# Performance work log

Measured on AMD Instinct MI355X. Metric: run time of the kernel, lower is better.

Reference implementation:

```python
import jax, jax.numpy as jnp
import numpy as np

B, S, D, H = 4, 2048, 1024, 16
DK = D // H
SCALE = 1.0 / np.float32(np.sqrt(DK))


def setup_inputs() -> dict:
    key = jax.random.key(0)
    ks = jax.random.split(key, 11)
    w = lambda k: (jax.random.normal(k, (D, D), jnp.float32) * 0.02)
    b = lambda k: (jax.random.normal(k, (D,), jnp.float32) * 0.02)
    return {
        "Q": jax.random.normal(ks[0], (B, S, D), jnp.float32),
        "K": jax.random.normal(ks[1], (B, S, D), jnp.float32),
        "V": jax.random.normal(ks[2], (B, S, D), jnp.float32),
        "Wq": w(ks[3]), "bq": b(ks[4]),
        "Wk": w(ks[5]), "bk": b(ks[6]),
        "Wv": w(ks[7]), "bv": b(ks[8]),
        "Wo": w(ks[9]), "bo": b(ks[10]),
        # causal mask, broadcast over batch and heads: [1,1,S,S]
        "mask": jnp.tril(jnp.ones((1, 1, S, S), dtype=bool)),
    }


def reference(Q, K, V, Wq, bq, Wk, bk, Wv, bv, Wo, bo, mask):
    def proj(x, W, bias):
        # [B,S,D] -> [B,H,S,DK]
        return (x @ W + bias).reshape(B, S, H, DK).transpose(0, 2, 1, 3)

    q = proj(Q, Wq, bq)
    k = proj(K, Wk, bk)
    v = proj(V, Wv, bv)
    scores = jnp.einsum("bhqd,bhkd->bhqk", q, k) * SCALE  # [B,H,S,S]
    scores = jnp.where(mask, scores, jnp.float32(-1e9))
    attn = jax.nn.softmax(scores, axis=-1)
    out = jnp.einsum("bhqk,bhkd->bhqd", attn, v)  # [B,H,S,DK]
    out = out.transpose(0, 2, 1, 3).reshape(B, S, D)
    return out @ Wo + bo
```

## Files before the change

kernel.cpp:

```cpp
#include <hip/hip_runtime.h>
#include <hip/hip_bf16.h>
#include <stdint.h>

#define BB 4
#define SS 2048
#define DD 1024
#define HH 16
#define DKK 64
#define MM (BB * SS)

typedef __hip_bfloat16 bf16;
typedef __attribute__((ext_vector_type(8))) short frag8;
typedef __attribute__((ext_vector_type(4))) float f32x4;

#define GLDS16(g, l)                                                        \
  __builtin_amdgcn_global_load_lds(                                         \
      (const __attribute__((address_space(1))) void*)(g),                   \
      (__attribute__((address_space(3))) void*)(l), 16, 0, 0)

#define MFMA __builtin_amdgcn_mfma_f32_16x16x32_bf16

__device__ __forceinline__ unsigned short f2bu(float f) {
  __hip_bfloat16 h = __float2bfloat16(f);
  return *reinterpret_cast<unsigned short*>(&h);
}

struct WtArgs {
  const float* s[3];
  unsigned short* d[3];
};
__global__ __launch_bounds__(256) void wtrans_kernel(WtArgs a) {
  const float* __restrict__ W = a.s[blockIdx.z];
  unsigned short* __restrict__ Wt = a.d[blockIdx.z];
  __shared__ float t[64][68];
  const int n0 = blockIdx.x * 64, k0 = blockIdx.y * 64;
  const int tid = threadIdx.x;
#pragma unroll
  for (int it = 0; it < 4; ++it) {
    const int kk = it * 16 + (tid >> 4);
    const int nn = (tid & 15) * 4;
    const float4 v = *(const float4*)&W[(size_t)(k0 + kk) * DD + n0 + nn];
    *(float4*)&t[kk][nn] = v;
  }
  __syncthreads();
#pragma unroll
  for (int it = 0; it < 2; ++it) {
    const int n = it * 32 + (tid >> 3);
    const int c = tid & 7;
    frag8 pk;
#pragma unroll
    for (int j = 0; j < 8; ++j) pk[j] = (short)f2bu(t[c * 8 + j][n]);
    *(frag8*)&Wt[(size_t)(n0 + n) * DD + k0 + c * 8] = pk;
  }
}

template <int A_BF16, int OUT_MODE>
__global__ __launch_bounds__(256) void gemm_kernel(
    const void* __restrict__ Av, const unsigned short* __restrict__ Wt,
    const float* __restrict__ bias, void* __restrict__ outv, float oscale) {
  constexpr int K = DD;
  __shared__ unsigned short Bs[128 * 64];
  __shared__ unsigned short As[128 * 64];
  const int tid = threadIdx.x;
  const int wave = tid >> 6, lane = tid & 63, quad = lane >> 4, l15 = lane & 15;
  const int wr = wave >> 1, wc = wave & 1;
  const int m0 = blockIdx.y * 128, n0 = blockIdx.x * 128;

  f32x4 acc[4][4] = {};

  for (int k0 = 0; k0 < K; k0 += 64) {
#pragma unroll
    for (int c = 0; c < 4; ++c) {
      const int row = c * 32 + wave * 8 + (lane >> 3);
      const int gc = ((lane & 7) ^ (row & 7)) * 8;
      const unsigned short* g = &Wt[(size_t)(n0 + row) * K + k0 + gc];
      unsigned off = __builtin_amdgcn_readfirstlane(
          (unsigned)((c * 32 + wave * 8) * 128));
      GLDS16(g, (char*)&Bs[0] + off);
    }
    if (A_BF16) {
      const unsigned short* A = (const unsigned short*)Av;
#pragma unroll
      for (int c = 0; c < 4; ++c) {
        const int row = c * 32 + wave * 8 + (lane >> 3);
        const int gc = ((lane & 7) ^ (row & 7)) * 8;
        const unsigned short* g = &A[(size_t)(m0 + row) * K + k0 + gc];
        unsigned off = __builtin_amdgcn_readfirstlane(
            (unsigned)((c * 32 + wave * 8) * 128));
        GLDS16(g, (char*)&As[0] + off);
      }
    } else {
      const float* A = (const float*)Av;
#pragma unroll
      for (int it = 0; it < 4; ++it) {
        const int row = it * 32 + (tid >> 3);
        const int c = tid & 7;
        const float4 v0 = *(const float4*)&A[(size_t)(m0 + row) * K + k0 + c * 8];
        const float4 v1 =
            *(const float4*)&A[(size_t)(m0 + row) * K + k0 + c * 8 + 4];
        frag8 pk;
        pk[0] = (short)f2bu(v0.x); pk[1] = (short)f2bu(v0.y);
        pk[2] = (short)f2bu(v0.z); pk[3] = (short)f2bu(v0.w);
        pk[4] = (short)f2bu(v1.x); pk[5] = (short)f2bu(v1.y);
        pk[6] = (short)f2bu(v1.z); pk[7] = (short)f2bu(v1.w);
        *(frag8*)&As[row * 64 + ((c ^ (row & 7)) * 8)] = pk;
      }
    }
    __syncthreads();

#pragma unroll
    for (int s = 0; s < 2; ++s) {
      frag8 af[4], bfr[4];
#pragma unroll
      for (int mi = 0; mi < 4; ++mi)
        af[mi] = *(const frag8*)
            &As[(wr * 64 + mi * 16 + l15) * 64 + (((s * 4 + quad) ^ (l15 & 7)) * 8)];
#pragma unroll
      for (int ni = 0; ni < 4; ++ni)
        bfr[ni] = *(const frag8*)
            &Bs[(wc * 64 + ni * 16 + l15) * 64 + (((s * 4 + quad) ^ (l15 & 7)) * 8)];
#pragma unroll
      for (int mi = 0; mi < 4; ++mi)
#pragma unroll
        for (int ni = 0; ni < 4; ++ni)
          acc[mi][ni] = MFMA(af[mi], bfr[ni], acc[mi][ni], 0, 0, 0);
    }
    __syncthreads();
  }

#pragma unroll
  for (int mi = 0; mi < 4; ++mi) {
#pragma unroll
    for (int ni = 0; ni < 4; ++ni) {
#pragma unroll
      for (int r = 0; r < 4; ++r) {
        const int grow = m0 + wr * 64 + mi * 16 + quad * 4 + r;
        const int gcol = n0 + wc * 64 + ni * 16 + l15;
        const float val = (acc[mi][ni][r] + bias[gcol]) * oscale;
        if (OUT_MODE == 2) {
          ((float*)outv)[(size_t)grow * DD + gcol] = val;
        } else {
          const int b = grow / SS, s = grow % SS;
          const int h = gcol / DKK, dk = gcol % DKK;
          unsigned short* o = (unsigned short*)outv;
          if (OUT_MODE == 0)
            o[(((size_t)(b * HH + h)) * SS + s) * DKK + dk] = f2bu(val);
          else
            o[(((size_t)(b * HH + h)) * DKK + dk) * SS + s] = f2bu(val);
        }
      }
    }
  }
}

__global__ __launch_bounds__(256) void fattn_kernel(
    const unsigned short* __restrict__ q, const unsigned short* __restrict__ k,
    const unsigned short* __restrict__ vt, unsigned short* __restrict__ ctx) {
  __shared__ unsigned short Ks[2][64 * 64];
  __shared__ unsigned short Vs[2][64 * 64];
  __shared__ unsigned short P_lds[4][16][36];
  const int tid = threadIdx.x;
  const int wave = tid >> 6, lane = tid & 63, quad = lane >> 4, l15 = lane & 15;
  const int bh = blockIdx.x & 63;
  const int tp = blockIdx.x >> 6;
  const size_t qkb = (size_t)bh * SS * DKK;
  const size_t vtb = (size_t)bh * DKK * SS;
  const int b = bh / HH, h = bh % HH;

  frag8 ones;
#pragma unroll
  for (int s = 0; s < 8; ++s) ones[s] = (short)0x3F80;

  auto stage = [&](int buf, int jt) {
#pragma unroll
    for (int c = 0; c < 2; ++c) {
      const int row = wave * 16 + c * 8 + (lane >> 3);
      const int gc = ((lane & 7) ^ (row & 7)) * 8;
      const unsigned short* g = &k[qkb + (size_t)(jt * 64 + row) * DKK + gc];
      unsigned off = __builtin_amdgcn_readfirstlane(
          (unsigned)(buf * 8192 + (wave * 16 + c * 8) * 128));
      GLDS16(g, (char*)&Ks[0][0] + off);
    }
#pragma unroll
    for (int c = 0; c < 2; ++c) {
      const int row = wave * 16 + c * 8 + (lane >> 3);
      const int gc = ((lane & 7) ^ (row & 7)) * 8;
      const unsigned short* g = &vt[vtb + (size_t)row * SS + jt * 64 + gc];
      unsigned off = __builtin_amdgcn_readfirstlane(
          (unsigned)(buf * 8192 + (wave * 16 + c * 8) * 128));
      GLDS16(g, (char*)&Vs[0][0] + off);
    }
  };

  for (int half = 0; half < 2; ++half) {
    const int t = half ? (31 - tp) : tp;
    const int q0 = t * 64 + wave * 16;

    const frag8 aq0 =
        *(const frag8*)&q[qkb + (size_t)(q0 + l15) * DKK + quad * 8];
    const frag8 aq1 =
        *(const frag8*)&q[qkb + (size_t)(q0 + l15) * DKK + 32 + quad * 8];

    f32x4 oacc[4] = {};
    f32x4 lacc = {};

    const int nT = t + 1;
    stage(0, 0);
    __syncthreads();

    for (int jt = 0; jt < nT; ++jt) {
      const int p = jt & 1;
      if (jt + 1 < nT) stage(1 - p, jt + 1);
      const bool diag = (jt == t);

#pragma unroll
      for (int jsub = 0; jsub < 2; ++jsub) {
        f32x4 sc[2];
#pragma unroll
        for (int g = 0; g < 2; ++g) {
          const int row = jsub * 32 + g * 16 + l15;
          const frag8 kf0 =
              *(const frag8*)&Ks[p][row * 64 + ((quad ^ (l15 & 7)) * 8)];
          const frag8 kf1 =
              *(const frag8*)&Ks[p][row * 64 + (((4 + quad) ^ (l15 & 7)) * 8)];
          f32x4 z = {};
          z = MFMA(aq0, kf0, z, 0, 0, 0);
          sc[g] = MFMA(aq1, kf1, z, 0, 0, 0);
        }
        float p0[4], p1[4];
        if (diag) {
          const int jg = jt * 64 + jsub * 32;
#pragma unroll
          for (int r = 0; r < 4; ++r) {
            const int ig = q0 + quad * 4 + r;
            p0[r] = (jg + l15 <= ig) ? __expf(sc[0][r]) : 0.f;
            p1[r] = (jg + 16 + l15 <= ig) ? __expf(sc[1][r]) : 0.f;
          }
        } else {
#pragma unroll
          for (int r = 0; r < 4; ++r) {
            p0[r] = __expf(sc[0][r]);
            p1[r] = __expf(sc[1][r]);
          }
        }
#pragma unroll
        for (int r = 0; r < 4; ++r) {
          P_lds[wave][quad * 4 + r][l15] = f2bu(p0[r]);
          P_lds[wave][quad * 4 + r][16 + l15] = f2bu(p1[r]);
        }
        const frag8 pa = *(const frag8*)&P_lds[wave][l15][quad * 8];
#pragma unroll
        for (int c = 0; c < 4; ++c) {
          const int vrow = c * 16 + l15;
          const int chunk = ((jsub * 4 + quad) ^ (l15 & 7));
          const frag8 vf = *(const frag8*)&Vs[p][vrow * 64 + chunk * 8];
          oacc[c] = MFMA(pa, vf, oacc[c], 0, 0, 0);
        }
        lacc = MFMA(pa, ones, lacc, 0, 0, 0);
      }
      __syncthreads();
    }

#pragma unroll
    for (int r = 0; r < 4; ++r) {
      const float inv = 1.f / lacc[r];
      const int ig = q0 + quad * 4 + r;
#pragma unroll
      for (int c = 0; c < 4; ++c)
        ctx[((size_t)(b * SS + ig)) * DD + h * DKK + c * 16 + l15] =
            f2bu(oacc[c][r] * inv);
    }
  }
}

extern "C" void kernel_launch(void* const* d_in, const int* in_sizes, int n_in,
                              void* d_out, int out_size, void* d_ws,
                              size_t ws_size, hipStream_t stream) {
  const float* Q = (const float*)d_in[0];
  const float* K = (const float*)d_in[1];
  const float* V = (const float*)d_in[2];
  const float* Wq = (const float*)d_in[3];
  const float* bq = (const float*)d_in[4];
  const float* Wk = (const float*)d_in[5];
  const float* bk = (const float*)d_in[6];
  const float* Wv = (const float*)d_in[7];
  const float* bv = (const float*)d_in[8];
  const float* Wo = (const float*)d_in[9];
  const float* bo = (const float*)d_in[10];

  const size_t NE = (size_t)MM * DD;
  unsigned short* ctx = (unsigned short*)d_ws;
  unsigned short* qp = ctx + NE;
  unsigned short* kp = qp + NE;
  unsigned short* vtp = kp + NE;
  unsigned short* Wqt = ctx;
  unsigned short* Wkt = ctx + 1048576;
  unsigned short* Wvt = ctx + 2097152;
  unsigned short* Wot = qp;

  const dim3 gg(DD / 128, MM / 128);

  WtArgs wa1;
  wa1.s[0] = Wq; wa1.s[1] = Wk; wa1.s[2] = Wv;
  wa1.d[0] = Wqt; wa1.d[1] = Wkt; wa1.d[2] = Wvt;
  wtrans_kernel<<<dim3(16, 16, 3), 256, 0, stream>>>(wa1);

  gemm_kernel<0, 0><<<gg, 256, 0, stream>>>((const void*)Q, Wqt, bq, qp,
                                            0.125f);
  gemm_kernel<0, 0><<<gg, 256, 0, stream>>>((const void*)K, Wkt, bk, kp, 1.f);
  gemm_kernel<0, 1><<<gg, 256, 0, stream>>>((const void*)V, Wvt, bv, vtp, 1.f);

  fattn_kernel<<<dim3(BB * HH * 16), 256, 0, stream>>>(qp, kp, vtp, ctx);

  WtArgs wa2;
  wa2.s[0] = Wo; wa2.d[0] = Wot;
  wa2.s[1] = Wo; wa2.d[1] = Wot;
  wa2.s[2] = Wo; wa2.d[2] = Wot;
  wtrans_kernel<<<dim3(16, 16, 1), 256, 0, stream>>>(wa2);

  gemm_kernel<1, 2><<<gg, 256, 0, stream>>>((const void*)ctx, Wot, bo,
                                            (void*)d_out, 1.f);
}
```

Before: 376.2 us.

## Batch QKV projections into one launch and pre-convert inputs to bf16

Merges the three Q/K/V projection GEMMs into a single launch that uses blockIdx.z to pick per-projection arguments, and makes the output mode a runtime value. When the workspace is large enough, a separate kernel first converts Q/K/V to bf16, so the GEMM can use its bf16 A-loading path, and all four weight transposes run in one launch. This cuts launch count and lets the projection GEMM pull half-width A tiles. In exchange the conversion adds an extra read and write pass over the activations, and a runtime branch replaces the compile-time output mode.

```diff
diff --git a/kernel.cpp b/kernel.cpp
--- a/kernel.cpp
+++ b/kernel.cpp
@@ -25,9 +25,27 @@
   return *reinterpret_cast<unsigned short*>(&h);
 }
 
-struct WtArgs {
+struct CvtArgs {
   const float* s[3];
   unsigned short* d[3];
+};
+__global__ __launch_bounds__(256) void cvt_kernel(CvtArgs a) {
+  const float* __restrict__ s = a.s[blockIdx.z];
+  unsigned short* __restrict__ d = a.d[blockIdx.z];
+  const size_t i = ((size_t)blockIdx.x * 256 + threadIdx.x) * 8;
+  const float4 v0 = *(const float4*)&s[i];
+  const float4 v1 = *(const float4*)&s[i + 4];
+  frag8 pk;
+  pk[0] = (short)f2bu(v0.x); pk[1] = (short)f2bu(v0.y);
+  pk[2] = (short)f2bu(v0.z); pk[3] = (short)f2bu(v0.w);
+  pk[4] = (short)f2bu(v1.x); pk[5] = (short)f2bu(v1.y);
+  pk[6] = (short)f2bu(v1.z); pk[7] = (short)f2bu(v1.w);
+  *(frag8*)&d[i] = pk;
+}
+
+struct WtArgs {
+  const float* s[4];
+  unsigned short* d[4];
 };
 __global__ __launch_bounds__(256) void wtrans_kernel(WtArgs a) {
   const float* __restrict__ W = a.s[blockIdx.z];
@@ -54,13 +72,27 @@
   }
 }
 
-template <int A_BF16, int OUT_MODE>
-__global__ __launch_bounds__(256) void gemm_kernel(
-    const void* __restrict__ Av, const unsigned short* __restrict__ Wt,
-    const float* __restrict__ bias, void* __restrict__ outv, float oscale) {
+struct GemmArgs {
+  const void* A[3];
+  const unsigned short* Wt[3];
+  const float* bias[3];
+  void* out[3];
+  float oscale[3];
+  int mode[3];
+};
+template <int A_BF16>
+__global__ __launch_bounds__(256) void gemm_kernel(GemmArgs ga) {
   constexpr int K = DD;
   __shared__ unsigned short Bs[128 * 64];
   __shared__ unsigned short As[128 * 64];
+  const int z = blockIdx.z;
+  const void* __restrict__ Av = ga.A[z];
+  const unsigned short* __restrict__ Wt = ga.Wt[z];
+  const float* __restrict__ bias = ga.bias[z];
+  void* __restrict__ outv = ga.out[z];
+  const float oscale = ga.oscale[z];
+  const int mode = ga.mode[z];
+
   const int tid = threadIdx.x;
   const int wave = tid >> 6, lane = tid & 63, quad = lane >> 4, l15 = lane & 15;
   const int wr = wave >> 1, wc = wave & 1;
@@ -137,13 +169,13 @@
         const int grow = m0 + wr * 64 + mi * 16 + quad * 4 + r;
         const int gcol = n0 + wc * 64 + ni * 16 + l15;
         const float val = (acc[mi][ni][r] + bias[gcol]) * oscale;
-        if (OUT_MODE == 2) {
+        if (mode == 2) {
           ((float*)outv)[(size_t)grow * DD + gcol] = val;
         } else {
           const int b = grow / SS, s = grow % SS;
           const int h = gcol / DKK, dk = gcol % DKK;
           unsigned short* o = (unsigned short*)outv;
-          if (OUT_MODE == 0)
+          if (mode == 0)
             o[(((size_t)(b * HH + h)) * SS + s) * DKK + dk] = f2bu(val);
           else
             o[(((size_t)(b * HH + h)) * DKK + dk) * SS + s] = f2bu(val);
@@ -289,35 +321,93 @@
   const float* bo = (const float*)d_in[10];
 
   const size_t NE = (size_t)MM * DD;
-  unsigned short* ctx = (unsigned short*)d_ws;
-  unsigned short* qp = ctx + NE;
-  unsigned short* kp = qp + NE;
-  unsigned short* vtp = kp + NE;
-  unsigned short* Wqt = ctx;
-  unsigned short* Wkt = ctx + 1048576;
-  unsigned short* Wvt = ctx + 2097152;
-  unsigned short* Wot = qp;
-
-  const dim3 gg(DD / 128, MM / 128);
-
-  WtArgs wa1;
-  wa1.s[0] = Wq; wa1.s[1] = Wk; wa1.s[2] = Wv;
-  wa1.d[0] = Wqt; wa1.d[1] = Wkt; wa1.d[2] = Wvt;
-  wtrans_kernel<<<dim3(16, 16, 3), 256, 0, stream>>>(wa1);
-
-  gemm_kernel<0, 0><<<gg, 256, 0, stream>>>((const void*)Q, Wqt, bq, qp,
-                                            0.125f);
-  gemm_kernel<0, 0><<<gg, 256, 0, stream>>>((const void*)K, Wkt, bk, kp, 1.f);
-  gemm_kernel<0, 1><<<gg, 256, 0, stream>>>((const void*)V, Wvt, bv, vtp, 1.f);
-
-  fattn_kernel<<<dim3(BB * HH * 16), 256, 0, stream>>>(qp, kp, vtp, ctx);
-
-  WtArgs wa2;
-  wa2.s[0] = Wo; wa2.d[0] = Wot;
-  wa2.s[1] = Wo; wa2.d[1] = Wot;
-  wa2.s[2] = Wo; wa2.d[2] = Wot;
-  wtrans_kernel<<<dim3(16, 16, 1), 256, 0, stream>>>(wa2);
-
-  gemm_kernel<1, 2><<<gg, 256, 0, stream>>>((const void*)ctx, Wot, bo,
-                                            (void*)d_out, 1.f);
-}
+  const dim3 gg(DD / 128, MM / 128, 3);
+  const dim3 gg1(DD / 128, MM / 128, 1);
+
+  const bool big = ws_size >= (size_t)110 * 1024 * 1024;
+
+  if (big) {
+    unsigned short* qb16 = (unsigned short*)d_ws;
+    unsigned short* kb16 = qb16 + NE;
+    unsigned short* vb16 = kb16 + NE;
+    unsigned short* qp = vb16 + NE;
+    unsigned short* kp = qp + NE;
+    unsigned short* vtp = kp + NE;
+    unsigned short* Wqt = vtp + NE;
+    unsigned short* Wkt = Wqt + (size_t)DD * DD;
+    unsigned short* Wvt = Wkt + (size_t)DD * DD;
+    unsigned short* Wot = Wvt + (size_t)DD * DD;
+    unsigned short* ctx = qb16;
+
+    WtArgs wa;
+    wa.s[0] = Wq; wa.s[1] = Wk; wa.s[2] = Wv; wa.s[3] = Wo;
+    wa.d[0] = Wqt; wa.d[1] = Wkt; wa.d[2] = Wvt; wa.d[3] = Wot;
+    wtrans_kernel<<<dim3(16, 16, 4), 256, 0, stream>>>(wa);
+
+    CvtArgs ca;
+    ca.s[0] = Q; ca.s[1] = K; ca.s[2] = V;
+    ca.d[0] = qb16; ca.d[1] = kb16; ca.d[2] = vb16;
+    cvt_kernel<<<dim3(4096, 1, 3), 256, 0, stream>>>(ca);
+
+    GemmArgs g1;
+    g1.A[0] = qb16; g1.A[1] = kb16; g1.A[2] = vb16;
+    g1.Wt[0] = Wqt; g1.Wt[1] = Wkt; g1.Wt[2] = Wvt;
+    g1.bias[0] = bq; g1.bias[1] = bk; g1.bias[2] = bv;
+    g1.out[0] = qp; g1.out[1] = kp; g1.out[2] = vtp;
+    g1.oscale[0] = 0.125f; g1.oscale[1] = 1.f; g1.oscale[2] = 1.f;
+    g1.mode[0] = 0; g1.mode[1] = 0; g1.mode[2] = 1;
+    gemm_kernel<1><<<gg, 256, 0, stream>>>(g1);
+
+    fattn_kernel<<<dim3(BB * HH * 16), 256, 0, stream>>>(qp, kp, vtp, ctx);
+
+    GemmArgs g2;
+    g2.A[0] = ctx; g2.Wt[0] = Wot; g2.bias[0] = bo; g2.out[0] = d_out;
+    g2.oscale[0] = 1.f; g2.mode[0] = 2;
+    g2.A[1] = g2.A[0]; g2.Wt[1] = g2.Wt[0]; g2.bias[1] = g2.bias[0];
+    g2.out[1] = g2.out[0]; g2.oscale[1] = 1.f; g2.mode[1] = 2;
+    g2.A[2] = g2.A[0]; g2.Wt[2] = g2.Wt[0]; g2.bias[2] = g2.bias[0];
+    g2.out[2] = g2.out[0]; g2.oscale[2] = 1.f; g2.mode[2] = 2;
+    gemm_kernel<1><<<gg1, 256, 0, stream>>>(g2);
+  } else {
+    unsigned short* ctx = (unsigned short*)d_ws;
+    unsigned short* qp = ctx + NE;
+    unsigned short* kp = qp + NE;
+    unsigned short* vtp = kp + NE;
+    unsigned short* Wqt = ctx;
+    unsigned short* Wkt = ctx + (size_t)DD * DD;
+    unsigned short* Wvt = ctx + 2 * (size_t)DD * DD;
+    unsigned short* Wot = qp;
+
+    WtArgs wa;
+    wa.s[0] = Wq; wa.s[1] = Wk; wa.s[2] = Wv; wa.s[3] = Wq;
+    wa.d[0] = Wqt; wa.d[1] = Wkt; wa.d[2] = Wvt; wa.d[3] = Wqt;
+    wtrans_kernel<<<dim3(16, 16, 3), 256, 0, stream>>>(wa);
+
+    GemmArgs g1;
+    g1.A[0] = Q; g1.A[1] = K; g1.A[2] = V;
+    g1.Wt[0] = Wqt; g1.Wt[1] = Wkt; g1.Wt[2] = Wvt;
+    g1.bias[0] = bq; g1.bias[1] = bk; g1.bias[2] = bv;
+    g1.out[0] = qp; g1.out[1] = kp; g1.out[2] = vtp;
+    g1.oscale[0] = 0.125f; g1.oscale[1] = 1.f; g1.oscale[2] = 1.f;
+    g1.mode[0] = 0; g1.mode[1] = 0; g1.mode[2] = 1;
+    gemm_kernel<0><<<gg, 256, 0, stream>>>(g1);
+
+    fattn_kernel<<<dim3(BB * HH * 16), 256, 0, stream>>>(qp, kp, vtp, ctx);
+
+    WtArgs wb;
+    wb.s[0] = Wo; wb.d[0] = Wot;
+    wb.s[1] = Wo; wb.d[1] = Wot;
+    wb.s[2] = Wo; wb.d[2] = Wot;
+    wb.s[3] = Wo; wb.d[3] = Wot;
+    wtrans_kernel<<<dim3(16, 16, 1), 256, 0, stream>>>(wb);
+
+    GemmArgs g2;
+    g2.A[0] = ctx; g2.Wt[0] = Wot; g2.bias[0] = bo; g2.out[0] = d_out;
+    g2.oscale[0] = 1.f; g2.mode[0] = 2;
+    g2.A[1] = g2.A[0]; g2.Wt[1] = g2.Wt[0]; g2.bias[1] = g2.bias[0];
+    g2.out[1] = g2.out[0]; g2.oscale[1] = 1.f; g2.mode[1] = 2;
+    g2.A[2] = g2.A[0]; g2.Wt[2] = g2.Wt[0]; g2.bias[2] = g2.bias[0];
+    g2.out[2] = g2.out[0]; g2.oscale[2] = 1.f; g2.mode[2] = 2;
+    gemm_kernel<1><<<gg1, 256, 0, stream>>>(g2);
+  }
+}
```

Result: no change. 379.1 us (+0.8%).
